# Optimization experiments

Measured on AMD Instinct MI355X. Metric: run time of the kernel, lower is better.

The kernel has to match this reference:

```python
import jax, jax.numpy as jnp
import numpy as np

D_MODEL, D_K, D_V, H, GRID = 512, 64, 64, 8, 196
B = 4


def setup_inputs() -> dict:
    key = jax.random.key(0)
    ks = jax.random.split(key, 12)
    s = 0.02
    return {
        "queries": jax.random.normal(ks[0], (B, GRID, D_MODEL), jnp.float32),
        "keys": jax.random.normal(ks[1], (B, GRID, D_MODEL), jnp.float32),
        "values": jax.random.normal(ks[2], (B, GRID, D_MODEL), jnp.float32),
        "Wq": jax.random.normal(ks[3], (H * D_K, D_MODEL), jnp.float32) * s,
        "bq": jnp.zeros((H * D_K,), jnp.float32),
        "Wk": jax.random.normal(ks[4], (H * D_K, D_MODEL), jnp.float32) * s,
        "bk": jnp.zeros((H * D_K,), jnp.float32),
        "Wv": jax.random.normal(ks[5], (H * D_V, D_MODEL), jnp.float32) * s,
        "bv": jnp.zeros((H * D_V,), jnp.float32),
        "Wo": jax.random.normal(ks[6], (D_MODEL, H * D_V), jnp.float32) * s,
        "bo": jnp.zeros((D_MODEL,), jnp.float32),
        "scale": jnp.ones((1, H, GRID, GRID), jnp.float32) / np.sqrt(D_K).astype(np.float32),
    }


def reference(queries, keys, values, Wq, bq, Wk, bk, Wv, bv, Wo, bo, scale):
    b, nq, _ = queries.shape
    nk = values.shape[1]
    # linear projections (torch nn.Linear: x @ W.T + b)
    q_sig = queries @ Wq.T + bq          # (b, nq, h*dk)
    k_p = keys @ Wk.T + bk               # (b, nk, h*dk)
    v_p = values @ Wv.T + bv             # (b, nk, h*dv)
    # elementwise q*k interaction (b, nq, nk, h*dk)
    att_e = q_sig[:, :, None, :] * k_p[:, None, :, :]
    # sigmoid-gated values
    v_g = jax.nn.sigmoid(att_e) * v_p[:, None, :, :]
    v = v_g.reshape(b, nq, nk, H, D_K).transpose(0, 3, 1, 2, 4)      # (b,h,nq,nk,dk)
    att = att_e.reshape(b, nq, nk, H, D_K).transpose(0, 3, 1, 2, 4)  # (b,h,nq,nk,dk)
    att = att.sum(-1) * scale            # (b,h,nq,nk)
    p = jax.nn.softmax(att, axis=-1)     # dropout is identity in eval mode
    # (att.unsqueeze(-2) @ v).squeeze(-2)
    image = jnp.einsum("bhqk,bhqkd->bhqd", p, v)
    image = image.transpose(0, 2, 1, 3).reshape(b, nq, H * D_V)
    out = image @ Wo.T + bo              # (b, nq, d_model)
    out = jax.nn.sigmoid(q_sig * out) * out
    return out
```

## Files before the change

### kernel.cpp

```cpp
#include <hip/hip_runtime.h>
#include <hip/hip_bf16.h>
#include <math.h>

#define NQ 196
#define BATCH 4
#define HD 512
#define NH 8
#define DK 64
#define MROWS 784
#define MPAD 832

typedef __attribute__((ext_vector_type(8))) short short8;
typedef __attribute__((ext_vector_type(4))) short short4v;
typedef __attribute__((ext_vector_type(4))) float float4v;

__device__ __forceinline__ float b2f(short s) {
  return __uint_as_float(((unsigned)(unsigned short)s) << 16);
}
__device__ __forceinline__ short f2b(float x) {
  return __builtin_bit_cast(short, __float2bfloat16(x));
}
__device__ __forceinline__ float fexp2(float x) {
  float r; asm("v_exp_f32 %0, %1" : "=v"(r) : "v"(x)); return r;
}
__device__ __forceinline__ float frcp(float x) {
  float r; asm("v_rcp_f32 %0, %1" : "=v"(r) : "v"(x)); return r;
}
__device__ __forceinline__ void cvt4(float4 v, short4v& hi, short4v& lo) {
  float x[4] = {v.x, v.y, v.z, v.w};
  #pragma unroll
  for (int i = 0; i < 4; ++i) {
    hi[i] = f2b(x[i]);
    lo[i] = f2b(x[i] - b2f(hi[i]));
  }
}
__device__ __forceinline__ void gload_lds16(const void* g, void* l) {
  __builtin_amdgcn_global_load_lds(
      (const __attribute__((address_space(1))) unsigned int*)g,
      (__attribute__((address_space(3))) unsigned int*)l, 16, 0, 0);
}

struct WSplitArgs { const float* src[4]; short* hi[4]; short* lo[4]; };

__global__ __launch_bounds__(256)
void wsplit_kernel(WSplitArgs a) {
  const int seg = blockIdx.x >> 7;
  const size_t off = (size_t)(blockIdx.x & 127) * 2048 + (size_t)threadIdx.x * 8;
  const float* src = a.src[seg] + off;
  float4 v0 = *(const float4*)(src);
  float4 v1 = *(const float4*)(src + 4);
  short4v h0, l0, h1, l1;
  cvt4(v0, h0, l0); cvt4(v1, h1, l1);
  short8 vh = {h0[0],h0[1],h0[2],h0[3],h1[0],h1[1],h1[2],h1[3]};
  short8 vl = {l0[0],l0[1],l0[2],l0[3],l1[0],l1[1],l1[2],l1[3]};
  *(short8*)(a.hi[seg] + off) = vh;
  *(short8*)(a.lo[seg] + off) = vl;
}

struct GemmArgs {
  const float* X[3]; const short* Wh[3]; const short* Wl[3]; const float* bias[3];
  float* Cf[3]; short* Ch[3]; short* Cl[3]; const float* gate[3];
};

__global__ __launch_bounds__(512)
void mgemm(GemmArgs p, int N, int K) {
  const int z = blockIdx.z;
  const float* __restrict__ X  = p.X[z];
  const short* __restrict__ Wh = p.Wh[z];
  const short* __restrict__ Wl = p.Wl[z];

  __shared__ short smem[20480];
  short* const A_ = smem;
  short* const B_ = smem + 4096;
  float* const redC = (float*)smem;

  const int t = threadIdx.x;
  const int g = t >> 8;
  const int tt = t & 255;
  const int ln = t & 63, lm = ln & 15, quad = ln >> 4;
  const int w = (t >> 6) & 3;
  const int m0 = blockIdx.x * 16, n0 = blockIdx.y * 64;
  const int kb = g << 8;

  const int aRow = (tt & 127) >> 3, aK = (tt & 7) << 2;
  const bool aload = tt < 128;
  const float* Ap = X + (size_t)(m0 + aRow) * K + kb + aK;
  const int aIdx = aRow * 32 + aK;
  const int bRow = tt >> 2, bK = (tt & 3) << 3;
  const short* Bph = Wh + (size_t)(n0 + bRow) * K + kb + bK;
  const short* Bpl = Wl + (size_t)(n0 + bRow) * K + kb + bK;

  const int wn = w << 4;
  float4v acc = {0.f, 0.f, 0.f, 0.f};

  const int T = 8;
  float4 ra = aload ? *(const float4*)Ap : make_float4(0.f,0.f,0.f,0.f);
  gload_lds16(Bph, &B_[(((g << 1) + 0) * 2 + 0) * 2048 + tt * 8]);
  gload_lds16(Bpl, &B_[(((g << 1) + 0) * 2 + 1) * 2048 + tt * 8]);
  if (aload) {
    short4v ahi, alo; cvt4(ra, ahi, alo);
    *(short4v*)&A_[(((g << 1) + 0) * 2 + 0) * 512 + aIdx] = ahi;
    *(short4v*)&A_[(((g << 1) + 0) * 2 + 1) * 512 + aIdx] = alo;
  }

  for (int kt = 0; kt < T; ++kt) {
    const int buf = kt & 1;
    __syncthreads();
    if (kt + 1 < T) {
      if (aload) ra = *(const float4*)(Ap + (size_t)(kt + 1) * 32);
      const int nb = buf ^ 1;
      gload_lds16(Bph + (size_t)(kt + 1) * 32, &B_[(((g << 1) + nb) * 2 + 0) * 2048 + tt * 8]);
      gload_lds16(Bpl + (size_t)(kt + 1) * 32, &B_[(((g << 1) + nb) * 2 + 1) * 2048 + tt * 8]);
    }
    const short* Ab = &A_[((g << 1) + buf) * 2 * 512];
    const short* Bb = &B_[((g << 1) + buf) * 2 * 2048];
    short8 fah = *(const short8*)&Ab[0 * 512 + lm * 32 + (quad << 3)];
    short8 fal = *(const short8*)&Ab[1 * 512 + lm * 32 + (quad << 3)];
    short8 fbh = *(const short8*)&Bb[0 * 2048 + (wn + lm) * 32 + (quad << 3)];
    short8 fbl = *(const short8*)&Bb[1 * 2048 + (wn + lm) * 32 + (quad << 3)];
    acc = __builtin_amdgcn_mfma_f32_16x16x32_bf16(fah, fbh, acc, 0,0,0);
    acc = __builtin_amdgcn_mfma_f32_16x16x32_bf16(fah, fbl, acc, 0,0,0);
    acc = __builtin_amdgcn_mfma_f32_16x16x32_bf16(fal, fbh, acc, 0,0,0);
    if (kt + 1 < T) {
      const int nb = buf ^ 1;
      if (aload) {
        short4v ahi, alo; cvt4(ra, ahi, alo);
        *(short4v*)&A_[(((g << 1) + nb) * 2 + 0) * 512 + aIdx] = ahi;
        *(short4v*)&A_[(((g << 1) + nb) * 2 + 1) * 512 + aIdx] = alo;
      }
    }
  }

  __syncthreads();
  if (g == 1) *(float4v*)&redC[tt * 4] = acc;
  __syncthreads();
  if (g == 0) {
    const float* bias = p.bias[z];
    const float* gate = p.gate[z];
    float* Cf = p.Cf[z]; short* Ch = p.Ch[z]; short* Cl = p.Cl[z];
    const int n = n0 + wn + lm;
    const float bv = bias[n];
    #pragma unroll
    for (int r = 0; r < 4; ++r) {
      const int m = m0 + (quad << 2) + r;
      float c = acc[r] + redC[tt * 4 + r] + bv;
      if (gate) {
        const float qg = gate[(size_t)m * N + n];
        c = __fdividef(c, 1.f + __expf(-qg * c));
      }
      if (Cf) Cf[(size_t)m * N + n] = c;
      if (Ch) {
        const short hi = f2b(c);
        Ch[(size_t)m * N + n] = hi;
        Cl[(size_t)m * N + n] = f2b(c - b2f(hi));
      }
    }
  }
}

__global__ __launch_bounds__(512)
void attn_fused(const short* __restrict__ qsh, const short* __restrict__ qsl,
                const short* __restrict__ ksh, const short* __restrict__ ksl,
                const float* __restrict__ qsg, const float* __restrict__ kpg,
                const float* __restrict__ vpg, const float* __restrict__ scg,
                float* __restrict__ img) {
  const int q0 = blockIdx.x * 16;
  const int h  = blockIdx.y;
  const int b  = blockIdx.z;
  const int t  = threadIdx.x;
  const int w = t >> 6, ln = t & 63;
  const int lm = ln & 15, quad = ln >> 4;
  const float L2E = 1.4426950408889634f;

  __shared__ float S[16][210];
  __shared__ float R[8][16][64];

  const size_t abase = ((size_t)(b * NQ) + q0 + lm) * HD + h * DK + (quad << 3);
  short8 ah0 = *(const short8*)(qsh + abase);
  short8 ah1 = *(const short8*)(qsh + abase + 32);
  short8 al0 = *(const short8*)(qsl + abase);
  short8 al1 = *(const short8*)(qsl + abase + 32);

  for (int nt = w; nt < 13; nt += 8) {
    const size_t bbase = ((size_t)(b * NQ) + nt * 16 + lm) * HD + h * DK + (quad << 3);
    short8 bh0 = *(const short8*)(ksh + bbase);
    short8 bh1 = *(const short8*)(ksh + bbase + 32);
    short8 bl0 = *(const short8*)(ksl + bbase);
    short8 bl1 = *(const short8*)(ksl + bbase + 32);
    float4v acc = {0.f, 0.f, 0.f, 0.f};
    acc = __builtin_amdgcn_mfma_f32_16x16x32_bf16(ah0, bh0, acc, 0,0,0);
    acc = __builtin_amdgcn_mfma_f32_16x16x32_bf16(ah1, bh1, acc, 0,0,0);
    acc = __builtin_amdgcn_mfma_f32_16x16x32_bf16(ah0, bl0, acc, 0,0,0);
    acc = __builtin_amdgcn_mfma_f32_16x16x32_bf16(ah1, bl1, acc, 0,0,0);
    acc = __builtin_amdgcn_mfma_f32_16x16x32_bf16(al0, bh0, acc, 0,0,0);
    acc = __builtin_amdgcn_mfma_f32_16x16x32_bf16(al1, bh1, acc, 0,0,0);
    #pragma unroll
    for (int r = 0; r < 4; ++r)
      S[(quad << 2) + r][nt * 16 + lm] = acc[r];
  }
  __syncthreads();

  for (int i = 0; i < 2; ++i) {
    const int rr = (w << 1) + i;
    const int q = q0 + rr;
    const bool qok = q < NQ;
    const float* srow = scg + ((size_t)h * NQ + (qok ? q : 0)) * NQ;
    float att[4];
    #pragma unroll
    for (int j = 0; j < 4; ++j) {
      const int c = ln + (j << 6);
      att[j] = -1e30f;
      if (c < NQ) att[j] = S[rr][c] * srow[c] * L2E;
    }
    float m = fmaxf(fmaxf(att[0], att[1]), fmaxf(att[2], att[3]));
    #pragma unroll
    for (int off = 32; off; off >>= 1) m = fmaxf(m, __shfl_xor(m, off, 64));
    float e[4], s = 0.f;
    #pragma unroll
    for (int j = 0; j < 4; ++j) { e[j] = fexp2(att[j] - m); s += e[j]; }
    #pragma unroll
    for (int off = 32; off; off >>= 1) s += __shfl_xor(s, off, 64);
    const float rinv = __fdividef(1.f, s);
    #pragma unroll
    for (int j = 0; j < 4; ++j) {
      const int c = ln + (j << 6);
      if (c < NQ) S[rr][c] = e[j] * rinv;
    }
  }
  __syncthreads();

  const int d = ln;
  const int kg = w;
  const int kbeg = (kg * 49) >> 1;
  const int kend = ((kg + 1) * 49) >> 1;
  const float LOG2E = 1.4426950408889634f;

  float nqs[16];
  #pragma unroll
  for (int qi = 0; qi < 16; ++qi) {
    const int row = min(b * NQ + q0 + qi, MROWS - 1);
    nqs[qi] = -qsg[(size_t)row * HD + h * DK + d] * LOG2E;
  }
  const float* kp = kpg + ((size_t)(b * NQ)) * HD + h * DK + d;
  const float* vp = vpg + ((size_t)(b * NQ)) * HD + h * DK + d;

  float acc[16];
  #pragma unroll
  for (int qi = 0; qi < 16; ++qi) acc[qi] = 0.f;

  for (int k = kbeg; k < kend; ++k) {
    const float kv = kp[(size_t)k * HD];
    const float vv = vp[(size_t)k * HD];
    #pragma unroll
    for (int qi = 0; qi < 16; ++qi) {
      const float e = fexp2(nqs[qi] * kv);
      const float g = vv * frcp(1.f + e);
      acc[qi] += S[qi][k] * g;
    }
  }
  #pragma unroll
  for (int qi = 0; qi < 16; ++qi) R[kg][qi][d] = acc[qi];
  __syncthreads();

  #pragma unroll
  for (int j = 0; j < 2; ++j) {
    const int idx = t + (j << 9);
    const int qi = idx >> 6, dd = idx & 63;
    const int q = q0 + qi;
    if (q < NQ) {
      float s = 0.f;
      #pragma unroll
      for (int kk = 0; kk < 8; ++kk) s += R[kk][qi][dd];
      img[((size_t)(b * NQ) + q) * HD + h * DK + dd] = s;
    }
  }
}

extern "C" void kernel_launch(void* const* d_in, const int* in_sizes, int n_in,
                              void* d_out, int out_size, void* d_ws, size_t ws_size,
                              hipStream_t stream) {
  const float* queries = (const float*)d_in[0];
  const float* keys    = (const float*)d_in[1];
  const float* values  = (const float*)d_in[2];
  const float* Wq = (const float*)d_in[3];
  const float* bq = (const float*)d_in[4];
  const float* Wk = (const float*)d_in[5];
  const float* bk = (const float*)d_in[6];
  const float* Wv = (const float*)d_in[7];
  const float* bv = (const float*)d_in[8];
  const float* Wo = (const float*)d_in[9];
  const float* bo = (const float*)d_in[10];
  const float* scale = (const float*)d_in[11];

  char* base = (char*)d_ws;
  const size_t FB = sizeof(float);
  const size_t NELF  = (size_t)MROWS * HD;
  const size_t NELPS = (size_t)MPAD * HD;
  const size_t WEL   = (size_t)HD * HD;

  size_t o = 0;
  float* q_sig = (float*)(base + o); o += NELF * FB;
  float* k_p   = (float*)(base + o); o += NELF * FB;
  float* v_p   = (float*)(base + o); o += NELF * FB;
  float* image = (float*)(base + o); o += NELF * FB;
  short* qsh = (short*)(base + o); o += NELPS * 2;
  short* qsl = (short*)(base + o); o += NELPS * 2;
  short* ksh = (short*)(base + o); o += NELPS * 2;
  short* ksl = (short*)(base + o); o += NELPS * 2;
  short* Wqh = (short*)(base + o); o += WEL * 2;
  short* Wql = (short*)(base + o); o += WEL * 2;
  short* Wkh = (short*)(base + o); o += WEL * 2;
  short* Wkl = (short*)(base + o); o += WEL * 2;
  short* Wvh = (short*)(base + o); o += WEL * 2;
  short* Wvl = (short*)(base + o); o += WEL * 2;
  short* Woh = (short*)(base + o); o += WEL * 2;
  short* Wol = (short*)(base + o); o += WEL * 2;

  WSplitArgs wa;
  wa.src[0] = Wq; wa.hi[0] = Wqh; wa.lo[0] = Wql;
  wa.src[1] = Wk; wa.hi[1] = Wkh; wa.lo[1] = Wkl;
  wa.src[2] = Wv; wa.hi[2] = Wvh; wa.lo[2] = Wvl;
  wa.src[3] = Wo; wa.hi[3] = Woh; wa.lo[3] = Wol;
  wsplit_kernel<<<512, 256, 0, stream>>>(wa);

  GemmArgs gp;
  gp.X[0] = queries; gp.Wh[0] = Wqh; gp.Wl[0] = Wql; gp.bias[0] = bq;
  gp.Cf[0] = q_sig;  gp.Ch[0] = qsh; gp.Cl[0] = qsl; gp.gate[0] = nullptr;
  gp.X[1] = keys;    gp.Wh[1] = Wkh; gp.Wl[1] = Wkl; gp.bias[1] = bk;
  gp.Cf[1] = k_p;    gp.Ch[1] = ksh; gp.Cl[1] = ksl; gp.gate[1] = nullptr;
  gp.X[2] = values;  gp.Wh[2] = Wvh; gp.Wl[2] = Wvl; gp.bias[2] = bv;
  gp.Cf[2] = v_p;    gp.Ch[2] = nullptr; gp.Cl[2] = nullptr; gp.gate[2] = nullptr;
  mgemm<<<dim3(MROWS/16, HD/64, 3), 512, 0, stream>>>(gp, HD, HD);

  attn_fused<<<dim3(13, NH, BATCH), 512, 0, stream>>>(
      qsh, qsl, ksh, ksl, q_sig, k_p, v_p, scale, image);

  GemmArgs go;
  go.X[0] = image; go.Wh[0] = Woh; go.Wl[0] = Wol; go.bias[0] = bo;
  go.Cf[0] = (float*)d_out; go.Ch[0] = nullptr; go.Cl[0] = nullptr; go.gate[0] = q_sig;
  for (int i = 1; i < 3; ++i) {
    go.X[i] = nullptr; go.Wh[i] = nullptr; go.Wl[i] = nullptr; go.bias[i] = nullptr;
    go.Cf[i] = nullptr; go.Ch[i] = nullptr; go.Cl[i] = nullptr; go.gate[i] = nullptr;
  }
  mgemm<<<dim3(MROWS/16, HD/64, 1), 512, 0, stream>>>(go, HD, HD);
}
```

Measured before the change: 138.5 us.

## Fuse all stages into one cooperative persistent kernel with grid syncs

Replaces the weight-split, projection GEMM, attention and output GEMM launches with a single cooperative kernel of 416 blocks. The blocks step through the phases separated by grid-wide syncs and share a union of shared memory. This is meant to remove per-launch overhead and the gaps between kernels. In exchange it adds grid barrier cost and a grid-stride tile loop. If the cooperative launch fails, it falls back to four separate launches.

```diff
diff --git a/kernel.cpp b/kernel.cpp
--- a/kernel.cpp
+++ b/kernel.cpp
@@ -1,6 +1,9 @@
 #include <hip/hip_runtime.h>
+#include <hip/hip_cooperative_groups.h>
 #include <hip/hip_bf16.h>
 #include <math.h>
+
+namespace cg = cooperative_groups;
 
 #define NQ 196
 #define BATCH 4
@@ -9,6 +12,8 @@
 #define DK 64
 #define MROWS 784
 #define MPAD 832
+#define GRIDB 416
+#define NTHR 512
 
 typedef __attribute__((ext_vector_type(8))) short short8;
 typedef __attribute__((ext_vector_type(4))) short short4v;
@@ -40,36 +45,42 @@
       (__attribute__((address_space(3))) unsigned int*)l, 16, 0, 0);
 }
 
-struct WSplitArgs { const float* src[4]; short* hi[4]; short* lo[4]; };
-
-__global__ __launch_bounds__(256)
-void wsplit_kernel(WSplitArgs a) {
-  const int seg = blockIdx.x >> 7;
-  const size_t off = (size_t)(blockIdx.x & 127) * 2048 + (size_t)threadIdx.x * 8;
-  const float* src = a.src[seg] + off;
-  float4 v0 = *(const float4*)(src);
-  float4 v1 = *(const float4*)(src + 4);
-  short4v h0, l0, h1, l1;
-  cvt4(v0, h0, l0); cvt4(v1, h1, l1);
-  short8 vh = {h0[0],h0[1],h0[2],h0[3],h1[0],h1[1],h1[2],h1[3]};
-  short8 vl = {l0[0],l0[1],l0[2],l0[3],l1[0],l1[1],l1[2],l1[3]};
-  *(short8*)(a.hi[seg] + off) = vh;
-  *(short8*)(a.lo[seg] + off) = vl;
-}
-
-struct GemmArgs {
-  const float* X[3]; const short* Wh[3]; const short* Wl[3]; const float* bias[3];
-  float* Cf[3]; short* Ch[3]; short* Cl[3]; const float* gate[3];
+struct FusedArgs {
+  const float *queries, *keys, *values;
+  const float *Wq, *bq, *Wk, *bk, *Wv, *bv, *Wo, *bo, *scale;
+  float *q_sig, *k_p, *v_p, *image, *outp;
+  short *qsh, *qsl, *ksh, *ksl;
+  short *Wqh, *Wql, *Wkh, *Wkl, *Wvh, *Wvl, *Woh, *Wol;
 };
 
-__global__ __launch_bounds__(512)
-void mgemm(GemmArgs p, int N, int K) {
-  const int z = blockIdx.z;
-  const float* __restrict__ X  = p.X[z];
-  const short* __restrict__ Wh = p.Wh[z];
-  const short* __restrict__ Wl = p.Wl[z];
-
-  __shared__ short smem[20480];
+struct AttnSmem { float S[16][210]; float R[8][16][64]; };
+union SmemU { short gemm[20480]; AttnSmem at; };
+
+__device__ __forceinline__ void phase0_body(const FusedArgs& a, int bid) {
+  const int t = threadIdx.x;
+  for (unsigned idx = (unsigned)bid * NTHR + t; idx < 262144u;
+       idx += (unsigned)GRIDB * NTHR) {
+    const int seg = idx >> 16;
+    const size_t off = (size_t)(idx & 65535u) << 2;
+    const float* s; short* hh; short* ll;
+    if (seg == 0)      { s = a.Wq; hh = a.Wqh; ll = a.Wql; }
+    else if (seg == 1) { s = a.Wk; hh = a.Wkh; ll = a.Wkl; }
+    else if (seg == 2) { s = a.Wv; hh = a.Wvh; ll = a.Wvl; }
+    else               { s = a.Wo; hh = a.Woh; ll = a.Wol; }
+    float4 v = *(const float4*)(s + off);
+    short4v h, l; cvt4(v, h, l);
+    *(short4v*)(hh + off) = h;
+    *(short4v*)(ll + off) = l;
+  }
+}
+
+__device__ __forceinline__ void gemm_tile(
+    const float* __restrict__ X, const short* __restrict__ Wh,
+    const short* __restrict__ Wl, const float* __restrict__ bias,
+    const float* __restrict__ gate, float* __restrict__ Cf,
+    short* __restrict__ Ch, short* __restrict__ Cl,
+    int m0, int n0, short* smem) {
+  const int K = HD, N = HD;
   short* const A_ = smem;
   short* const B_ = smem + 4096;
   float* const redC = (float*)smem;
@@ -79,7 +90,6 @@
   const int tt = t & 255;
   const int ln = t & 63, lm = ln & 15, quad = ln >> 4;
   const int w = (t >> 6) & 3;
-  const int m0 = blockIdx.x * 16, n0 = blockIdx.y * 64;
   const int kb = g << 8;
 
   const int aRow = (tt & 127) >> 3, aK = (tt & 7) << 2;
@@ -94,7 +104,7 @@
   float4v acc = {0.f, 0.f, 0.f, 0.f};
 
   const int T = 8;
-  float4 ra = aload ? *(const float4*)Ap : make_float4(0.f,0.f,0.f,0.f);
+  float4 ra = aload ? *(const float4*)Ap : make_float4(0.f, 0.f, 0.f, 0.f);
   gload_lds16(Bph, &B_[(((g << 1) + 0) * 2 + 0) * 2048 + tt * 8]);
   gload_lds16(Bpl, &B_[(((g << 1) + 0) * 2 + 1) * 2048 + tt * 8]);
   if (aload) {
@@ -135,9 +145,6 @@
   if (g == 1) *(float4v*)&redC[tt * 4] = acc;
   __syncthreads();
   if (g == 0) {
-    const float* bias = p.bias[z];
-    const float* gate = p.gate[z];
-    float* Cf = p.Cf[z]; short* Ch = p.Ch[z]; short* Cl = p.Cl[z];
     const int n = n0 + wn + lm;
     const float bv = bias[n];
     #pragma unroll
@@ -156,37 +163,46 @@
       }
     }
   }
-}
-
-__global__ __launch_bounds__(512)
-void attn_fused(const short* __restrict__ qsh, const short* __restrict__ qsl,
-                const short* __restrict__ ksh, const short* __restrict__ ksl,
-                const float* __restrict__ qsg, const float* __restrict__ kpg,
-                const float* __restrict__ vpg, const float* __restrict__ scg,
-                float* __restrict__ img) {
-  const int q0 = blockIdx.x * 16;
-  const int h  = blockIdx.y;
-  const int b  = blockIdx.z;
+  __syncthreads();
+}
+
+__device__ __forceinline__ void proj_body(const FusedArgs& a, int bid, short* smem) {
+  for (int tile = bid; tile < 1176; tile += GRIDB) {
+    const int z = tile / 392;
+    const int r = tile - z * 392;
+    const int m0 = (r >> 3) << 4;
+    const int n0 = (r & 7) << 6;
+    const float* X; const short* Wh; const short* Wl; const float* bias;
+    float* Cf; short* Ch; short* Cl;
+    if (z == 0)      { X=a.queries; Wh=a.Wqh; Wl=a.Wql; bias=a.bq; Cf=a.q_sig; Ch=a.qsh; Cl=a.qsl; }
+    else if (z == 1) { X=a.keys;    Wh=a.Wkh; Wl=a.Wkl; bias=a.bk; Cf=a.k_p;   Ch=a.ksh; Cl=a.ksl; }
+    else             { X=a.values;  Wh=a.Wvh; Wl=a.Wvl; bias=a.bv; Cf=a.v_p;   Ch=nullptr; Cl=nullptr; }
+    gemm_tile(X, Wh, Wl, bias, nullptr, Cf, Ch, Cl, m0, n0, smem);
+  }
+}
+
+__device__ __forceinline__ void attn_body(const FusedArgs& a, int bid, AttnSmem& sm) {
+  const int qt = bid % 13;
+  const int h  = (bid / 13) % NH;
+  const int b  = bid / (13 * NH);
+  const int q0 = qt * 16;
   const int t  = threadIdx.x;
   const int w = t >> 6, ln = t & 63;
   const int lm = ln & 15, quad = ln >> 4;
   const float L2E = 1.4426950408889634f;
 
-  __shared__ float S[16][210];
-  __shared__ float R[8][16][64];
-
   const size_t abase = ((size_t)(b * NQ) + q0 + lm) * HD + h * DK + (quad << 3);
-  short8 ah0 = *(const short8*)(qsh + abase);
-  short8 ah1 = *(const short8*)(qsh + abase + 32);
-  short8 al0 = *(const short8*)(qsl + abase);
-  short8 al1 = *(const short8*)(qsl + abase + 32);
+  short8 ah0 = *(const short8*)(a.qsh + abase);
+  short8 ah1 = *(const short8*)(a.qsh + abase + 32);
+  short8 al0 = *(const short8*)(a.qsl + abase);
+  short8 al1 = *(const short8*)(a.qsl + abase + 32);
 
   for (int nt = w; nt < 13; nt += 8) {
     const size_t bbase = ((size_t)(b * NQ) + nt * 16 + lm) * HD + h * DK + (quad << 3);
-    short8 bh0 = *(const short8*)(ksh + bbase);
-    short8 bh1 = *(const short8*)(ksh + bbase + 32);
-    short8 bl0 = *(const short8*)(ksl + bbase);
-    short8 bl1 = *(const short8*)(ksl + bbase + 32);
+    short8 bh0 = *(const short8*)(a.ksh + bbase);
+    short8 bh1 = *(const short8*)(a.ksh + bbase + 32);
+    short8 bl0 = *(const short8*)(a.ksl + bbase);
+    short8 bl1 = *(const short8*)(a.ksl + bbase + 32);
     float4v acc = {0.f, 0.f, 0.f, 0.f};
     acc = __builtin_amdgcn_mfma_f32_16x16x32_bf16(ah0, bh0, acc, 0,0,0);
     acc = __builtin_amdgcn_mfma_f32_16x16x32_bf16(ah1, bh1, acc, 0,0,0);
@@ -196,7 +212,7 @@
     acc = __builtin_amdgcn_mfma_f32_16x16x32_bf16(al1, bh1, acc, 0,0,0);
     #pragma unroll
     for (int r = 0; r < 4; ++r)
-      S[(quad << 2) + r][nt * 16 + lm] = acc[r];
+      sm.S[(quad << 2) + r][nt * 16 + lm] = acc[r];
   }
   __syncthreads();
 
@@ -204,13 +220,13 @@
     const int rr = (w << 1) + i;
     const int q = q0 + rr;
     const bool qok = q < NQ;
-    const float* srow = scg + ((size_t)h * NQ + (qok ? q : 0)) * NQ;
+    const float* srow = a.scale + ((size_t)h * NQ + (qok ? q : 0)) * NQ;
     float att[4];
     #pragma unroll
     for (int j = 0; j < 4; ++j) {
       const int c = ln + (j << 6);
       att[j] = -1e30f;
-      if (c < NQ) att[j] = S[rr][c] * srow[c] * L2E;
+      if (c < NQ) att[j] = sm.S[rr][c] * srow[c] * L2E;
     }
     float m = fmaxf(fmaxf(att[0], att[1]), fmaxf(att[2], att[3]));
     #pragma unroll
@@ -224,7 +240,7 @@
     #pragma unroll
     for (int j = 0; j < 4; ++j) {
       const int c = ln + (j << 6);
-      if (c < NQ) S[rr][c] = e[j] * rinv;
+      if (c < NQ) sm.S[rr][c] = e[j] * rinv;
     }
   }
   __syncthreads();
@@ -239,10 +255,10 @@
   #pragma unroll
   for (int qi = 0; qi < 16; ++qi) {
     const int row = min(b * NQ + q0 + qi, MROWS - 1);
-    nqs[qi] = -qsg[(size_t)row * HD + h * DK + d] * LOG2E;
-  }
-  const float* kp = kpg + ((size_t)(b * NQ)) * HD + h * DK + d;
-  const float* vp = vpg + ((size_t)(b * NQ)) * HD + h * DK + d;
+    nqs[qi] = -a.q_sig[(size_t)row * HD + h * DK + d] * LOG2E;
+  }
+  const float* kp = a.k_p + ((size_t)(b * NQ)) * HD + h * DK + d;
+  const float* vp = a.v_p + ((size_t)(b * NQ)) * HD + h * DK + d;
 
   float acc[16];
   #pragma unroll
@@ -255,11 +271,11 @@
     for (int qi = 0; qi < 16; ++qi) {
       const float e = fexp2(nqs[qi] * kv);
       const float g = vv * frcp(1.f + e);
-      acc[qi] += S[qi][k] * g;
-    }
-  }
-  #pragma unroll
-  for (int qi = 0; qi < 16; ++qi) R[kg][qi][d] = acc[qi];
+      acc[qi] += sm.S[qi][k] * g;
+    }
+  }
+  #pragma unroll
+  for (int qi = 0; qi < 16; ++qi) sm.R[kg][qi][d] = acc[qi];
   __syncthreads();
 
   #pragma unroll
@@ -270,28 +286,58 @@
     if (q < NQ) {
       float s = 0.f;
       #pragma unroll
-      for (int kk = 0; kk < 8; ++kk) s += R[kk][qi][dd];
-      img[((size_t)(b * NQ) + q) * HD + h * DK + dd] = s;
-    }
-  }
+      for (int kk = 0; kk < 8; ++kk) s += sm.R[kk][qi][dd];
+      a.image[((size_t)(b * NQ) + q) * HD + h * DK + dd] = s;
+    }
+  }
+  __syncthreads();
+}
+
+__device__ __forceinline__ void out_body(const FusedArgs& a, int bid, short* smem) {
+  if (bid < 392) {
+    const int m0 = (bid >> 3) << 4;
+    const int n0 = (bid & 7) << 6;
+    gemm_tile(a.image, a.Woh, a.Wol, a.bo, a.q_sig, a.outp, nullptr, nullptr,
+              m0, n0, smem);
+  }
+}
+
+__global__ __launch_bounds__(NTHR, 4)
+void fused_all(FusedArgs a) {
+  __shared__ SmemU sm;
+  cg::grid_group grid = cg::this_grid();
+  const int bid = blockIdx.x;
+  phase0_body(a, bid);
+  __threadfence();
+  grid.sync();
+  proj_body(a, bid, sm.gemm);
+  __threadfence();
+  grid.sync();
+  attn_body(a, bid, sm.at);
+  __threadfence();
+  grid.sync();
+  out_body(a, bid, sm.gemm);
+}
+
+__global__ __launch_bounds__(NTHR, 4) void k_phase0(FusedArgs a) {
+  phase0_body(a, blockIdx.x);
+}
+__global__ __launch_bounds__(NTHR, 4) void k_proj(FusedArgs a) {
+  __shared__ SmemU sm;
+  proj_body(a, blockIdx.x, sm.gemm);
+}
+__global__ __launch_bounds__(NTHR, 4) void k_attn(FusedArgs a) {
+  __shared__ SmemU sm;
+  attn_body(a, blockIdx.x, sm.at);
+}
+__global__ __launch_bounds__(NTHR, 4) void k_out(FusedArgs a) {
+  __shared__ SmemU sm;
+  out_body(a, blockIdx.x, sm.gemm);
 }
 
 extern "C" void kernel_launch(void* const* d_in, const int* in_sizes, int n_in,
                               void* d_out, int out_size, void* d_ws, size_t ws_size,
                               hipStream_t stream) {
-  const float* queries = (const float*)d_in[0];
-  const float* keys    = (const float*)d_in[1];
-  const float* values  = (const float*)d_in[2];
-  const float* Wq = (const float*)d_in[3];
-  const float* bq = (const float*)d_in[4];
-  const float* Wk = (const float*)d_in[5];
-  const float* bk = (const float*)d_in[6];
-  const float* Wv = (const float*)d_in[7];
-  const float* bv = (const float*)d_in[8];
-  const float* Wo = (const float*)d_in[9];
-  const float* bo = (const float*)d_in[10];
-  const float* scale = (const float*)d_in[11];
-
   char* base = (char*)d_ws;
   const size_t FB = sizeof(float);
   const size_t NELF  = (size_t)MROWS * HD;
@@ -299,48 +345,41 @@
   const size_t WEL   = (size_t)HD * HD;
 
   size_t o = 0;
-  float* q_sig = (float*)(base + o); o += NELF * FB;
-  float* k_p   = (float*)(base + o); o += NELF * FB;
-  float* v_p   = (float*)(base + o); o += NELF * FB;
-  float* image = (float*)(base + o); o += NELF * FB;
-  short* qsh = (short*)(base + o); o += NELPS * 2;
-  short* qsl = (short*)(base + o); o += NELPS * 2;
-  short* ksh = (short*)(base + o); o += NELPS * 2;
-  short* ksl = (short*)(base + o); o += NELPS * 2;
-  short* Wqh = (short*)(base + o); o += WEL * 2;
-  short* Wql = (short*)(base + o); o += WEL * 2;
-  short* Wkh = (short*)(base + o); o += WEL * 2;
-  short* Wkl = (short*)(base + o); o += WEL * 2;
-  short* Wvh = (short*)(base + o); o += WEL * 2;
-  short* Wvl = (short*)(base + o); o += WEL * 2;
-  short* Woh = (short*)(base + o); o += WEL * 2;
-  short* Wol = (short*)(base + o); o += WEL * 2;
-
-  WSplitArgs wa;
-  wa.src[0] = Wq; wa.hi[0] = Wqh; wa.lo[0] = Wql;
-  wa.src[1] = Wk; wa.hi[1] = Wkh; wa.lo[1] = Wkl;
-  wa.src[2] = Wv; wa.hi[2] = Wvh; wa.lo[2] = Wvl;
-  wa.src[3] = Wo; wa.hi[3] = Woh; wa.lo[3] = Wol;
-  wsplit_kernel<<<512, 256, 0, stream>>>(wa);
-
-  GemmArgs gp;
-  gp.X[0] = queries; gp.Wh[0] = Wqh; gp.Wl[0] = Wql; gp.bias[0] = bq;
-  gp.Cf[0] = q_sig;  gp.Ch[0] = qsh; gp.Cl[0] = qsl; gp.gate[0] = nullptr;
-  gp.X[1] = keys;    gp.Wh[1] = Wkh; gp.Wl[1] = Wkl; gp.bias[1] = bk;
-  gp.Cf[1] = k_p;    gp.Ch[1] = ksh; gp.Cl[1] = ksl; gp.gate[1] = nullptr;
-  gp.X[2] = values;  gp.Wh[2] = Wvh; gp.Wl[2] = Wvl; gp.bias[2] = bv;
-  gp.Cf[2] = v_p;    gp.Ch[2] = nullptr; gp.Cl[2] = nullptr; gp.gate[2] = nullptr;
-  mgemm<<<dim3(MROWS/16, HD/64, 3), 512, 0, stream>>>(gp, HD, HD);
-
-  attn_fused<<<dim3(13, NH, BATCH), 512, 0, stream>>>(
-      qsh, qsl, ksh, ksl, q_sig, k_p, v_p, scale, image);
-
-  GemmArgs go;
-  go.X[0] = image; go.Wh[0] = Woh; go.Wl[0] = Wol; go.bias[0] = bo;
-  go.Cf[0] = (float*)d_out; go.Ch[0] = nullptr; go.Cl[0] = nullptr; go.gate[0] = q_sig;
-  for (int i = 1; i < 3; ++i) {
-    go.X[i] = nullptr; go.Wh[i] = nullptr; go.Wl[i] = nullptr; go.bias[i] = nullptr;
-    go.Cf[i] = nullptr; go.Ch[i] = nullptr; go.Cl[i] = nullptr; go.gate[i] = nullptr;
-  }
-  mgemm<<<dim3(MROWS/16, HD/64, 1), 512, 0, stream>>>(go, HD, HD);
-}
+  FusedArgs fa;
+  fa.queries = (const float*)d_in[0];
+  fa.keys    = (const float*)d_in[1];
+  fa.values  = (const float*)d_in[2];
+  fa.Wq = (const float*)d_in[3];  fa.bq = (const float*)d_in[4];
+  fa.Wk = (const float*)d_in[5];  fa.bk = (const float*)d_in[6];
+  fa.Wv = (const float*)d_in[7];  fa.bv = (const float*)d_in[8];
+  fa.Wo = (const float*)d_in[9];  fa.bo = (const float*)d_in[10];
+  fa.scale = (const float*)d_in[11];
+  fa.q_sig = (float*)(base + o); o += NELF * FB;
+  fa.k_p   = (float*)(base + o); o += NELF * FB;
+  fa.v_p   = (float*)(base + o); o += NELF * FB;
+  fa.image = (float*)(base + o); o += NELF * FB;
+  fa.qsh = (short*)(base + o); o += NELPS * 2;
+  fa.qsl = (short*)(base + o); o += NELPS * 2;
+  fa.ksh = (short*)(base + o); o += NELPS * 2;
+  fa.ksl = (short*)(base + o); o += NELPS * 2;
+  fa.Wqh = (short*)(base + o); o += WEL * 2;
+  fa.Wql = (short*)(base + o); o += WEL * 2;
+  fa.Wkh = (short*)(base + o); o += WEL * 2;
+  fa.Wkl = (short*)(base + o); o += WEL * 2;
+  fa.Wvh = (short*)(base + o); o += WEL * 2;
+  fa.Wvl = (short*)(base + o); o += WEL * 2;
+  fa.Woh = (short*)(base + o); o += WEL * 2;
+  fa.Wol = (short*)(base + o); o += WEL * 2;
+  fa.outp = (float*)d_out;
+
+  void* kp[] = {(void*)&fa};
+  hipError_t err = hipLaunchCooperativeKernel((const void*)fused_all,
+                                              dim3(GRIDB), dim3(NTHR),
+                                              kp, 0, stream);
+  if (err != hipSuccess) {
+    k_phase0<<<GRIDB, NTHR, 0, stream>>>(fa);
+    k_proj  <<<GRIDB, NTHR, 0, stream>>>(fa);
+    k_attn  <<<GRIDB, NTHR, 0, stream>>>(fa);
+    k_out   <<<GRIDB, NTHR, 0, stream>>>(fa);
+  }
+}
```

Measured after the change: 500.4 us. 261% more time.
